# Kernel tuning notes

Hardware: AMD Instinct MI355X
Metric: run time of the kernel (lower is better)

## Reference

```python
import jax, jax.numpy as jnp
import numpy as np

IMAGE_MAX_DIM = 1024
POOL = 7
NUM_CLASSES = 81
N_ROIS = 2000
BN_EPS = 1e-3


def _make_boxes(key, n):
    k1, k2, k3, k4 = jax.random.split(key, 4)
    cx = jax.random.uniform(k1, (n,), minval=0.0, maxval=IMAGE_MAX_DIM)
    cy = jax.random.uniform(k2, (n,), minval=0.0, maxval=IMAGE_MAX_DIM)
    w = jax.random.uniform(k3, (n,), minval=16.0, maxval=512.0)
    h = jax.random.uniform(k4, (n,), minval=16.0, maxval=512.0)
    x1 = jnp.clip(cx - w / 2, 0.0, IMAGE_MAX_DIM - 2.0)
    y1 = jnp.clip(cy - h / 2, 0.0, IMAGE_MAX_DIM - 2.0)
    x2 = jnp.clip(cx + w / 2, x1 + 1.0, IMAGE_MAX_DIM)
    y2 = jnp.clip(cy + h / 2, y1 + 1.0, IMAGE_MAX_DIM)
    return jnp.stack([x1, y1, x2, y2], axis=-1)[None]  # [1, n, 4]


def setup_inputs() -> dict:
    key = jax.random.key(0)
    ks = jax.random.split(key, 16)
    d = {
        'p2': jax.random.normal(ks[0], (1, 256, 256, 256), jnp.float32),
        'p3': jax.random.normal(ks[1], (1, 256, 128, 128), jnp.float32),
        'p4': jax.random.normal(ks[2], (1, 256, 64, 64), jnp.float32),
        'p5': jax.random.normal(ks[3], (1, 256, 32, 32), jnp.float32),
        'rpn_rois': _make_boxes(ks[4], N_ROIS),
        'conv1_w': jax.random.normal(ks[5], (1024, 256, POOL, POOL), jnp.float32) * 0.02,
        'conv1_b': jnp.zeros((1024,), jnp.float32),
        'bn1_g': jnp.ones((1024,), jnp.float32),
        'bn1_b': jnp.zeros((1024,), jnp.float32),
        'bn1_m': jnp.zeros((1024,), jnp.float32),
        'bn1_v': jnp.ones((1024,), jnp.float32),
        'conv2_w': jax.random.normal(ks[6], (1024, 1024), jnp.float32) * 0.02,
        'conv2_b': jnp.zeros((1024,), jnp.float32),
        'bn2_g': jnp.ones((1024,), jnp.float32),
        'bn2_b': jnp.zeros((1024,), jnp.float32),
        'bn2_m': jnp.zeros((1024,), jnp.float32),
        'bn2_v': jnp.ones((1024,), jnp.float32),
        'logits_w': jax.random.normal(ks[7], (NUM_CLASSES, 1024), jnp.float32) * 0.02,
        'logits_b': jnp.zeros((NUM_CLASSES,), jnp.float32),
        'bbox_w': jax.random.normal(ks[8], (NUM_CLASSES * 4, 1024), jnp.float32) * 0.02,
        'bbox_b': jnp.zeros((NUM_CLASSES * 4,), jnp.float32),
    }
    return d


def _crop_resize(fmap, boxes):
    """TF-style crop_and_resize, bilinear. fmap [C,H,W]; boxes [N,4] = (y1,x1,y2,x2) normalized."""
    C, H, W = fmap.shape
    dt = fmap.dtype
    y1, x1, y2, x2 = boxes[:, 0], boxes[:, 1], boxes[:, 2], boxes[:, 3]
    t = (jnp.arange(POOL, dtype=dt) / (POOL - 1))  # [P]
    ys = y1[:, None] * (H - 1) + t[None, :] * ((y2 - y1) * (H - 1))[:, None]  # [N,P]
    xs = x1[:, None] * (W - 1) + t[None, :] * ((x2 - x1) * (W - 1))[:, None]  # [N,P]
    y0 = jnp.floor(ys)
    x0 = jnp.floor(xs)
    ly = (ys - y0)[None, :, :, None]  # [1,N,P,1]
    lx = (xs - x0)[None, :, None, :]  # [1,N,1,P]
    y0i = jnp.clip(y0.astype(jnp.int32), 0, H - 1)
    y1i = jnp.clip(y0i + 1, 0, H - 1)
    x0i = jnp.clip(x0.astype(jnp.int32), 0, W - 1)
    x1i = jnp.clip(x0i + 1, 0, W - 1)

    def g(yi, xi):  # -> [C,N,P,P]
        return fmap[:, yi[:, :, None], xi[:, None, :]]

    out = (g(y0i, x0i) * (1 - ly) * (1 - lx) + g(y0i, x1i) * (1 - ly) * lx
           + g(y1i, x0i) * ly * (1 - lx) + g(y1i, x1i) * ly * lx)
    return jnp.transpose(out, (1, 0, 2, 3))  # [N,C,P,P]


def _forward(p2, p3, p4, p5, rpn_rois, conv1_w, conv1_b, bn1_g, bn1_b, bn1_m, bn1_v,
             conv2_w, conv2_b, bn2_g, bn2_b, bn2_m, bn2_v, logits_w, logits_b, bbox_w, bbox_b):
    rois = rpn_rois.reshape(-1, 4)  # [N,4] (x1,y1,x2,y2) in pixels
    x1, y1, x2, y2 = rois[:, 0], rois[:, 1], rois[:, 2], rois[:, 3]
    # level = clamp(round(log2(sqrt(area)/224)) + 4, 2, 5)
    roi_level = jnp.clip(jnp.round(jnp.log2(jnp.sqrt((y2 - y1) * (x2 - x1)) / 224.0)) + 4.0, 2.0, 5.0)
    boxes_n = (rois / float(IMAGE_MAX_DIM))[:, [1, 0, 3, 2]]  # (y1,x1,y2,x2) normalized

    pooled = jnp.zeros((rois.shape[0], 256, POOL, POOL), rois.dtype)
    for lvl, fmap in zip(range(2, 6), [p2, p3, p4, p5]):
        crops = _crop_resize(fmap[0], boxes_n)  # [N,256,P,P]
        mask = (roi_level == float(lvl))[:, None, None, None]
        pooled = pooled + jnp.where(mask, crops, 0.0)

    # conv1: 7x7 valid conv over [N,256,7,7] -> [N,1024]
    h = jnp.einsum('nchw,ochw->no', pooled, conv1_w) + conv1_b
    h = (h - bn1_m) * jax.lax.rsqrt(bn1_v + BN_EPS) * bn1_g + bn1_b
    h = jax.nn.relu(h)
    # conv2: 1x1 conv == matmul
    h = h @ conv2_w.T + conv2_b
    h = (h - bn2_m) * jax.lax.rsqrt(bn2_v + BN_EPS) * bn2_g + bn2_b
    shared = jax.nn.relu(h)  # [N,1024]

    logits = shared @ logits_w.T + logits_b
    probs = jax.nn.softmax(logits, axis=-1)
    bbox = shared @ bbox_w.T + bbox_b
    return (logits.reshape(1, N_ROIS, NUM_CLASSES),
            probs.reshape(1, N_ROIS, NUM_CLASSES),
            bbox.reshape(1, N_ROIS, NUM_CLASSES, 4))


def reference(p2, p3, p4, p5, rpn_rois, conv1_w, conv1_b, bn1_g, bn1_b, bn1_m, bn1_v,
              conv2_w, conv2_b, bn2_g, bn2_b, bn2_m, bn2_v, logits_w, logits_b, bbox_w, bbox_b):
    return _forward(p2, p3, p4, p5, rpn_rois, conv1_w, conv1_b, bn1_g, bn1_b, bn1_m, bn1_v,
                    conv2_w, conv2_b, bn2_g, bn2_b, bn2_m, bn2_v, logits_w, logits_b, bbox_w, bbox_b)
```

## Files before the change

### kernel.cpp

```cpp
#include <hip/hip_runtime.h>
#include <stdint.h>

#define NROI 2000
#define MPAD 2048
#define KP   12544
#define N1   1024
#define NCLS 81
#define NBOX 324
#define N3   405
#define N3P  448
#define BN_EPS 0.001f
#define KSPLIT 8

typedef __attribute__((ext_vector_type(8))) short bf16x8;
typedef __attribute__((ext_vector_type(4))) float f32x4;
typedef __attribute__((ext_vector_type(8))) unsigned short u16x8;

__device__ inline unsigned short f2bf(float f) {
  union { float f; unsigned u; } v; v.f = f;
  unsigned r = v.u + 0x7fffu + ((v.u >> 16) & 1u);
  return (unsigned short)(r >> 16);
}

__device__ inline float bf2f(unsigned short h) {
  union { unsigned u; float f; } v; v.u = (unsigned)h << 16; return v.f;
}

__device__ inline void gld16(const unsigned short* g, unsigned short* l) {
  __builtin_amdgcn_global_load_lds(
      (const __attribute__((address_space(1))) void*)g,
      (__attribute__((address_space(3))) void*)l, 16, 0, 0);
}

__device__ __forceinline__ void kslice(int kz, int& off, int& len) {
  if (kz < 4) { off = kz * 1536; len = 1536; }
  else        { off = 6144 + (kz - 4) * 1600; len = 1600; }
}

__global__ __launch_bounds__(256) void front_t(
    const float* __restrict__ p2, const float* __restrict__ p3,
    const float* __restrict__ p4, const float* __restrict__ p5,
    unsigned short* __restrict__ f2t, unsigned short* __restrict__ f3t,
    unsigned short* __restrict__ f4t, unsigned short* __restrict__ f5t) {
  int bb2 = blockIdx.x;
  int t = threadIdx.x;
  const float* src;
  unsigned short* dst;
  int HW;
  if (bb2 < 1024)      { src = p2; dst = f2t; HW = 65536; }
  else if (bb2 < 1280) { bb2 -= 1024; src = p3; dst = f3t; HW = 16384; }
  else if (bb2 < 1344) { bb2 -= 1280; src = p4; dst = f4t; HW = 4096; }
  else                 { bb2 -= 1344; src = p5; dst = f5t; HW = 1024; }
  int p0 = bb2 * 64;
  int lane = t & 63, w = t >> 6;
  int pq = (lane & 15) * 4;
  int cg = (lane >> 4) * 8;
#pragma unroll
  for (int it = 0; it < 2; ++it) {
    int c = w * 64 + it * 32 + cg;
    const float* sp = src + (size_t)c * HW + p0 + pq;
    float4 v[8];
#pragma unroll
    for (int k = 0; k < 8; ++k)
      v[k] = *(const float4*)(sp + (size_t)k * HW);
    unsigned short* dp = dst + (size_t)(p0 + pq) * 256 + c;
    u16x8 o0, o1, o2, o3;
#pragma unroll
    for (int k = 0; k < 8; ++k) {
      o0[k] = f2bf(v[k].x);
      o1[k] = f2bf(v[k].y);
      o2[k] = f2bf(v[k].z);
      o3[k] = f2bf(v[k].w);
    }
    *(u16x8*)(dp)       = o0;
    *(u16x8*)(dp + 256) = o1;
    *(u16x8*)(dp + 512) = o2;
    *(u16x8*)(dp + 768) = o3;
  }
}

__global__ __launch_bounds__(256) void roi_prep(
    const unsigned short* __restrict__ f2t, const unsigned short* __restrict__ f3t,
    const unsigned short* __restrict__ f4t, const unsigned short* __restrict__ f5t,
    const float* __restrict__ rois, unsigned short* __restrict__ pooled,
    const float* __restrict__ c1w, const float* __restrict__ c2w,
    const float* __restrict__ lw, const float* __restrict__ bw,
    const float* c1b, const float* g1, const float* b1, const float* m1, const float* v1,
    const float* c2b, const float* g2, const float* b2, const float* m2, const float* v2,
    const float* lb, const float* bb,
    unsigned short* __restrict__ w1p, unsigned short* __restrict__ w2b,
    unsigned short* __restrict__ w3b,
    float* s1, float* t1, float* s2, float* t2, float* b3) {
  __shared__ unsigned short srep[6272];
  int b = blockIdx.x;
  int t = threadIdx.x;
  if (b < 2048) {
    int n = b;
    int lane = t & 63, w = t >> 6;
    int c0 = lane * 4;
    unsigned short* out = pooled + (size_t)n * KP;
    if (n >= NROI) {
      for (int p = w; p < 49; p += 4)
        *(ushort4*)(out + p * 256 + c0) = make_ushort4(0, 0, 0, 0);
      return;
    }
    float x1 = rois[n * 4 + 0], y1 = rois[n * 4 + 1];
    float x2 = rois[n * 4 + 2], y2 = rois[n * 4 + 3];
    float area = (y2 - y1) * (x2 - x1);
    float lvl_f = rintf(log2f(sqrtf(area) / 224.0f)) + 4.0f;
    lvl_f = fminf(fmaxf(lvl_f, 2.0f), 5.0f);
    int lvl = (int)lvl_f;
    const unsigned short* f;
    int H;
    if (lvl == 2)      { f = f2t; H = 256; }
    else if (lvl == 3) { f = f3t; H = 128; }
    else if (lvl == 4) { f = f4t; H = 64;  }
    else               { f = f5t; H = 32;  }
    int W = H;
    const float inv = 1.0f / 1024.0f;
    float yn1 = y1 * inv, xn1 = x1 * inv, yn2 = y2 * inv, xn2 = x2 * inv;
    float hs = (yn2 - yn1) * (H - 1);
    float ws = (xn2 - xn1) * (W - 1);
    float yb = yn1 * (H - 1);
    float xb = xn1 * (W - 1);

    for (int p = w; p < 49; p += 4) {
      int py = p / 7, px = p - py * 7;
      float ysv = yb + ((float)py / 6.0f) * hs;
      float xsv = xb + ((float)px / 6.0f) * ws;
      float y0f = floorf(ysv), x0f = floorf(xsv);
      float ly = ysv - y0f, lx = xsv - x0f;
      int y0 = min(max((int)y0f, 0), H - 1);
      int y1i = min(y0 + 1, H - 1);
      int x0 = min(max((int)x0f, 0), W - 1);
      int x1i = min(x0 + 1, W - 1);
      ushort4 v00 = *(const ushort4*)(f + ((size_t)y0 * W + x0) * 256 + c0);
      ushort4 v01 = *(const ushort4*)(f + ((size_t)y0 * W + x1i) * 256 + c0);
      ushort4 v10 = *(const ushort4*)(f + ((size_t)y1i * W + x0) * 256 + c0);
      ushort4 v11 = *(const ushort4*)(f + ((size_t)y1i * W + x1i) * 256 + c0);
      ushort4 o;
      {
        float a = bf2f(v00.x), bq = bf2f(v01.x), cq = bf2f(v10.x), d = bf2f(v11.x);
        float top = a + lx * (bq - a), bot = cq + lx * (d - cq);
        o.x = f2bf(top + ly * (bot - top));
      }
      {
        float a = bf2f(v00.y), bq = bf2f(v01.y), cq = bf2f(v10.y), d = bf2f(v11.y);
        float top = a + lx * (bq - a), bot = cq + lx * (d - cq);
        o.y = f2bf(top + ly * (bot - top));
      }
      {
        float a = bf2f(v00.z), bq = bf2f(v01.z), cq = bf2f(v10.z), d = bf2f(v11.z);
        float top = a + lx * (bq - a), bot = cq + lx * (d - cq);
        o.z = f2bf(top + ly * (bot - top));
      }
      {
        float a = bf2f(v00.w), bq = bf2f(v01.w), cq = bf2f(v10.w), d = bf2f(v11.w);
        float top = a + lx * (bq - a), bot = cq + lx * (d - cq);
        o.w = f2bf(top + ly * (bot - top));
      }
      *(ushort4*)(out + p * 256 + c0) = o;
    }
  } else if (b < 4096) {
    int idx = b - 2048;
    int o = idx >> 1, h = idx & 1;
    const float4* src = (const float4*)(c1w + (size_t)o * KP + h * 6272);
    for (int k = t; k < 1568; k += 256) {
      float4 v = src[k];
      ushort4 q;
      q.x = f2bf(v.x); q.y = f2bf(v.y); q.z = f2bf(v.z); q.w = f2bf(v.w);
      *(ushort4*)&srep[k * 4] = q;
    }
    __syncthreads();
    unsigned short* dst = w1p + (size_t)o * KP + h * 128;
    int ch4 = (t & 31) * 4;
    int jw = t >> 5;
    for (int j = jw; j < 49; j += 8) {
      ushort4 q;
      q.x = srep[(ch4 + 0) * 49 + j];
      q.y = srep[(ch4 + 1) * 49 + j];
      q.z = srep[(ch4 + 2) * 49 + j];
      q.w = srep[(ch4 + 3) * 49 + j];
      *(ushort4*)(dst + j * 256 + ch4) = q;
    }
  } else if (b < 5120) {
    int j4 = (b - 4096) * 256 + t;
    float4 v = ((const float4*)c2w)[j4];
    ushort4 q;
    q.x = f2bf(v.x); q.y = f2bf(v.y); q.z = f2bf(v.z); q.w = f2bf(v.w);
    *(ushort4*)(w2b + (size_t)j4 * 4) = q;
  } else if (b < 5568) {
    int row = b - 5120;
    int k = t * 4;
    float4 v = {0.f, 0.f, 0.f, 0.f};
    if (row < NCLS)      v = *(const float4*)(lw + (size_t)row * 1024 + k);
    else if (row < N3)   v = *(const float4*)(bw + (size_t)(row - NCLS) * 1024 + k);
    ushort4 q;
    q.x = f2bf(v.x); q.y = f2bf(v.y); q.z = f2bf(v.z); q.w = f2bf(v.w);
    *(ushort4*)(w3b + (size_t)row * 1024 + k) = q;
  } else {
    for (int i = t; i < 1024; i += 256) {
      float sc = g1[i] * rsqrtf(v1[i] + BN_EPS);
      s1[i] = sc;
      t1[i] = (c1b[i] - m1[i]) * sc + b1[i];
      float ss = g2[i] * rsqrtf(v2[i] + BN_EPS);
      s2[i] = ss;
      t2[i] = (c2b[i] - m2[i]) * ss + b2[i];
    }
    for (int i = t; i < N3P; i += 256)
      b3[i] = (i < NCLS) ? lb[i] : (i < N3 ? bb[i - NCLS] : 0.0f);
  }
}

__global__ __launch_bounds__(512, 2) void gemm1_sk3(
    const unsigned short* __restrict__ A, const unsigned short* __restrict__ B,
    unsigned short* __restrict__ part) {
  __shared__ unsigned short AsF[4 * 8192];
  __shared__ unsigned short BsF[4 * 8192];
  int bid = blockIdx.x;
  int kz = bid & 7;
  int u = bid >> 3;
  int bn0 = (u & 3) * 256;
  int bm0 = (u >> 2) * 256;
  int koff, klen;
  kslice(kz, koff, klen);
  int nph = klen >> 5;

  int t = threadIdx.x;
  int lane = t & 63, w = t >> 6;
  int wr = w >> 2, wc = w & 3;
  int ln = lane & 15, q = lane >> 4;

  int clog = (lane & 3) ^ ((lane >> 3) & 3);
  int l4 = lane >> 2;
  const unsigned short* gA0 = A + (size_t)(bm0 + w * 32 + l4) * KP + koff + clog * 8;
  const unsigned short* gA1 = gA0 + (size_t)16 * KP;
  const unsigned short* gB0 = B + (size_t)(bn0 + w * 32 + l4) * KP + koff + clog * 8;
  const unsigned short* gB1 = gB0 + (size_t)16 * KP;
  int dc0 = (w * 128 + lane) * 8;
  int dc1 = dc0 + 64 * 8;

  int rxor = (q ^ ((ln >> 1) & 3)) * 8;
  int rdA = (wr * 128 + ln) * 32 + rxor;
  int rdB = (wc * 64 + ln) * 32 + rxor;

  f32x4 acc[8][4] = {};

#pragma unroll
  for (int ph = 0; ph < 3; ++ph) {
    int src = ph * 32;
    int db = ph * 8192;
    gld16(gA0 + src, AsF + db + dc0);
    gld16(gA1 + src, AsF + db + dc1);
    gld16(gB0 + src, BsF + db + dc0);
    gld16(gB1 + src, BsF + db + dc1);
  }
  asm volatile("s_waitcnt vmcnt(8)" ::: "memory");
  __builtin_amdgcn_s_barrier();
  asm volatile("" ::: "memory");

  for (int ph = 0; ph < nph; ++ph) {
    int rb = (ph & 3) * 8192;
    bf16x8 af[8], bfr[4];
#pragma unroll
    for (int mi = 0; mi < 8; ++mi)
      af[mi] = *(const bf16x8*)&AsF[rb + rdA + mi * 512];
#pragma unroll
    for (int nj = 0; nj < 4; ++nj)
      bfr[nj] = *(const bf16x8*)&BsF[rb + rdB + nj * 512];

    int phn = ph + 3;
    int src = (phn < nph) ? phn * 32 : 0;
    int db = (phn & 3) * 8192;
    gld16(gA0 + src, AsF + db + dc0);
    gld16(gA1 + src, AsF + db + dc1);
    gld16(gB0 + src, BsF + db + dc0);
    gld16(gB1 + src, BsF + db + dc1);

    __builtin_amdgcn_s_setprio(1);
#pragma unroll
    for (int mi = 0; mi < 8; ++mi)
#pragma unroll
      for (int nj = 0; nj < 4; ++nj)
        acc[mi][nj] = __builtin_amdgcn_mfma_f32_16x16x32_bf16(
            af[mi], bfr[nj], acc[mi][nj], 0, 0, 0);
    __builtin_amdgcn_s_setprio(0);

    asm volatile("s_waitcnt vmcnt(8)" ::: "memory");
    __builtin_amdgcn_s_barrier();
    asm volatile("" ::: "memory");
  }

  asm volatile("s_waitcnt vmcnt(0)" ::: "memory");

  unsigned short* po = part + (size_t)kz * MPAD * N1;
#pragma unroll
  for (int mi = 0; mi < 8; ++mi) {
    int m = bm0 + wr * 128 + mi * 16 + q * 4;
#pragma unroll
    for (int nj = 0; nj < 4; ++nj) {
      int n = bn0 + wc * 64 + nj * 16 + ln;
#pragma unroll
      for (int r = 0; r < 4; ++r)
        po[(size_t)(m + r) * N1 + n] = f2bf(acc[mi][nj][r]);
    }
  }
}

__global__ void reduce_sk(const unsigned short* __restrict__ part,
                          const float* __restrict__ sc, const float* __restrict__ sh,
                          unsigned short* __restrict__ outb) {
  const size_t P = (size_t)MPAD * N1;
  int m = blockIdx.x;
  int t = threadIdx.x;
  float4 v = {0.f, 0.f, 0.f, 0.f};
#pragma unroll
  for (int kz = 0; kz < KSPLIT; ++kz) {
    ushort4 u = *(const ushort4*)(part + kz * P + (size_t)m * N1 + t * 4);
    v.x += bf2f(u.x); v.y += bf2f(u.y); v.z += bf2f(u.z); v.w += bf2f(u.w);
  }
  int n0 = t * 4;
  ushort4 o;
  if (m < NROI) {
    o.x = f2bf(fmaxf(v.x * sc[n0 + 0] + sh[n0 + 0], 0.0f));
    o.y = f2bf(fmaxf(v.y * sc[n0 + 1] + sh[n0 + 1], 0.0f));
    o.z = f2bf(fmaxf(v.z * sc[n0 + 2] + sh[n0 + 2], 0.0f));
    o.w = f2bf(fmaxf(v.w * sc[n0 + 3] + sh[n0 + 3], 0.0f));
  } else {
    o = make_ushort4(0, 0, 0, 0);
  }
  *(ushort4*)(outb + (size_t)m * N1 + n0) = o;
}

template <int MODE>
__global__ __launch_bounds__(256) void gemm_bt(
    const unsigned short* __restrict__ A, const unsigned short* __restrict__ B,
    int M, int N, int K,
    const float* __restrict__ sc, const float* __restrict__ sh,
    unsigned short* __restrict__ outb, float* __restrict__ outf,
    int validM, int ldo) {
  __shared__ unsigned short As[64 * 64];
  __shared__ unsigned short Bs[64 * 64];
  int bm0 = blockIdx.y * 64;
  int bn0 = blockIdx.x * 64;
  int t = threadIdx.x;
  int lane = t & 63, w = t >> 6;
  int wm = (w & 1) * 32, wn = (w >> 1) * 32;
  int ln = lane & 15, q = lane >> 4;

  int r8 = t >> 3, j8 = t & 7;
  int sj = j8 ^ (r8 & 7);
  const unsigned short* ga = A + (size_t)(bm0 + r8) * K + sj * 8;
  const unsigned short* gb = B + (size_t)(bn0 + r8) * K + sj * 8;
  unsigned short* la = &As[t * 8];
  unsigned short* lb = &Bs[t * 8];
  int e = ln & 7;

  f32x4 acc00 = {0.f, 0.f, 0.f, 0.f}, acc01 = {0.f, 0.f, 0.f, 0.f};
  f32x4 acc10 = {0.f, 0.f, 0.f, 0.f}, acc11 = {0.f, 0.f, 0.f, 0.f};

  for (int k0 = 0; k0 < K; k0 += 64) {
    gld16(ga + k0, la);
    gld16(ga + k0 + (size_t)32 * K, la + 2048);
    gld16(gb + k0, lb);
    gld16(gb + k0 + (size_t)32 * K, lb + 2048);
    __syncthreads();
#pragma unroll
    for (int h = 0; h < 2; ++h) {
      int slot = ((h * 4 + q) ^ e) * 8;
      bf16x8 a0 = *(const bf16x8*)&As[(wm + ln) * 64 + slot];
      bf16x8 a1 = *(const bf16x8*)&As[(wm + 16 + ln) * 64 + slot];
      bf16x8 b0 = *(const bf16x8*)&Bs[(wn + ln) * 64 + slot];
      bf16x8 b1 = *(const bf16x8*)&Bs[(wn + 16 + ln) * 64 + slot];
      acc00 = __builtin_amdgcn_mfma_f32_16x16x32_bf16(a0, b0, acc00, 0, 0, 0);
      acc01 = __builtin_amdgcn_mfma_f32_16x16x32_bf16(a0, b1, acc01, 0, 0, 0);
      acc10 = __builtin_amdgcn_mfma_f32_16x16x32_bf16(a1, b0, acc10, 0, 0, 0);
      acc11 = __builtin_amdgcn_mfma_f32_16x16x32_bf16(a1, b1, acc11, 0, 0, 0);
    }
    __syncthreads();
  }

  f32x4 accs[2][2] = {{acc00, acc01}, {acc10, acc11}};
#pragma unroll
  for (int i = 0; i < 2; ++i)
#pragma unroll
    for (int j = 0; j < 2; ++j)
#pragma unroll
      for (int r = 0; r < 4; ++r) {
        int m = bm0 + wm + i * 16 + q * 4 + r;
        int n = bn0 + wn + j * 16 + ln;
        float v = accs[i][j][r];
        if (MODE == 1) {
          float o = fmaxf(v * sc[n] + sh[n], 0.0f);
          outb[(size_t)m * ldo + n] = (m < validM) ? f2bf(o) : (unsigned short)0;
        } else {
          outf[(size_t)m * ldo + n] = v + sh[n];
        }
      }
}

__global__ void head(const float* __restrict__ fc3, float* __restrict__ out) {
  int r = blockIdx.x;
  int t = threadIdx.x;
  const float* row = fc3 + (size_t)r * N3P;
  float v0 = (t < NCLS) ? row[t] : -INFINITY;
  float v1 = (t + 64 < NCLS) ? row[t + 64] : -INFINITY;
  float m = fmaxf(v0, v1);
#pragma unroll
  for (int o = 32; o > 0; o >>= 1) m = fmaxf(m, __shfl_xor(m, o, 64));
  float e0 = (t < NCLS) ? expf(v0 - m) : 0.0f;
  float e1 = (t + 64 < NCLS) ? expf(v1 - m) : 0.0f;
  float s = e0 + e1;
#pragma unroll
  for (int o = 32; o > 0; o >>= 1) s += __shfl_xor(s, o, 64);
  float invs = 1.0f / s;
  float* ol = out + (size_t)r * NCLS;
  float* op = out + 162000 + (size_t)r * NCLS;
  float* ob = out + 324000 + (size_t)r * NBOX;
  if (t < NCLS) { ol[t] = v0; op[t] = e0 * invs; }
  if (t + 64 < NCLS) { ol[t + 64] = v1; op[t + 64] = e1 * invs; }
  for (int j = t; j < NBOX; j += 64) ob[j] = row[NCLS + j];
}

extern "C" void kernel_launch(void* const* d_in, const int* in_sizes, int n_in,
                              void* d_out, int out_size, void* d_ws, size_t ws_size,
                              hipStream_t stream) {
  const float* p2  = (const float*)d_in[0];
  const float* p3  = (const float*)d_in[1];
  const float* p4  = (const float*)d_in[2];
  const float* p5  = (const float*)d_in[3];
  const float* roi = (const float*)d_in[4];
  const float* c1w = (const float*)d_in[5];
  const float* c1b = (const float*)d_in[6];
  const float* g1  = (const float*)d_in[7];
  const float* b1  = (const float*)d_in[8];
  const float* m1  = (const float*)d_in[9];
  const float* v1  = (const float*)d_in[10];
  const float* c2w = (const float*)d_in[11];
  const float* c2b = (const float*)d_in[12];
  const float* g2  = (const float*)d_in[13];
  const float* b2  = (const float*)d_in[14];
  const float* m2  = (const float*)d_in[15];
  const float* v2  = (const float*)d_in[16];
  const float* lw  = (const float*)d_in[17];
  const float* lb  = (const float*)d_in[18];
  const float* bw  = (const float*)d_in[19];
  const float* bb  = (const float*)d_in[20];
  float* out = (float*)d_out;

  char* ws = (char*)d_ws;
  size_t off = 0;
  auto alloc = [&](size_t bytes) {
    void* p = ws + off;
    off = (off + bytes + 255) & ~(size_t)255;
    return p;
  };
  unsigned short* pooled = (unsigned short*)alloc((size_t)MPAD * KP * 2);
  unsigned short* w1p    = (unsigned short*)alloc((size_t)N1 * KP * 2);
  unsigned short* w2b    = (unsigned short*)alloc((size_t)N1 * N1 * 2);
  unsigned short* w3b    = (unsigned short*)alloc((size_t)N3P * N1 * 2);
  unsigned short* a2     = (unsigned short*)alloc((size_t)MPAD * N1 * 2);
  unsigned short* shd    = (unsigned short*)alloc((size_t)MPAD * N1 * 2);
  float* fc3 = (float*)alloc((size_t)MPAD * N3P * 4);
  char* ub = (char*)alloc((size_t)48 * 1024 * 1024);
  unsigned short* f2t = (unsigned short*)ub;
  unsigned short* f3t = (unsigned short*)(ub + 33554432);
  unsigned short* f4t = (unsigned short*)(ub + 33554432 + 8388608);
  unsigned short* f5t = (unsigned short*)(ub + 33554432 + 8388608 + 2097152);
  unsigned short* part = (unsigned short*)ub;
  float* s1  = (float*)alloc(1024 * 4);
  float* t1  = (float*)alloc(1024 * 4);
  float* s2  = (float*)alloc(1024 * 4);
  float* t2  = (float*)alloc(1024 * 4);
  float* b3  = (float*)alloc(N3P * 4);

  front_t<<<1360, 256, 0, stream>>>(p2, p3, p4, p5, f2t, f3t, f4t, f5t);

  roi_prep<<<5569, 256, 0, stream>>>(f2t, f3t, f4t, f5t, roi, pooled,
                                     c1w, c2w, lw, bw,
                                     c1b, g1, b1, m1, v1, c2b, g2, b2, m2, v2,
                                     lb, bb,
                                     w1p, w2b, w3b, s1, t1, s2, t2, b3);

  gemm1_sk3<<<256, 512, 0, stream>>>(pooled, w1p, part);
  reduce_sk<<<MPAD, 256, 0, stream>>>(part, s1, t1, a2);

  gemm_bt<1><<<dim3(N1 / 64, MPAD / 64), 256, 0, stream>>>(
      a2, w2b, MPAD, N1, N1, s2, t2, shd, nullptr, NROI, N1);
  gemm_bt<2><<<dim3(N3P / 64, MPAD / 64), 256, 0, stream>>>(
      shd, w3b, MPAD, N3P, N1, nullptr, b3, nullptr, fc3, NROI, N3P);

  head<<<NROI, 64, 0, stream>>>(fc3, out);
}
```

Before: 309.7 us.

## Halve gemm1 M tile and shrink LDS ring to raise occupancy

The split-K conv1 GEMM moves from 256x256 tiles to 128x256 tiles, doubling the grid to 512 blocks. The LDS ring drops from 4 slots with 3-deep prefetch to 3 slots with 2-deep prefetch, and launch bounds ask for 4 blocks per CU. The goal is more resident blocks and better CU coverage across the 256 CUs. In exchange, B tiles are reloaded twice as often, each tile has lower arithmetic intensity, and there is less prefetch slack to hide memory latency.

```diff
diff --git a/kernel.cpp b/kernel.cpp
--- a/kernel.cpp
+++ b/kernel.cpp
@@ -212,16 +212,16 @@
   }
 }
 
-__global__ __launch_bounds__(512, 2) void gemm1_sk3(
+__global__ __launch_bounds__(512, 4) void gemm1_sk5(
     const unsigned short* __restrict__ A, const unsigned short* __restrict__ B,
     unsigned short* __restrict__ part) {
-  __shared__ unsigned short AsF[4 * 8192];
-  __shared__ unsigned short BsF[4 * 8192];
+  __shared__ unsigned short AsF[3 * 4096];
+  __shared__ unsigned short BsF[3 * 8192];
   int bid = blockIdx.x;
   int kz = bid & 7;
   int u = bid >> 3;
   int bn0 = (u & 3) * 256;
-  int bm0 = (u >> 2) * 256;
+  int bm0 = (u >> 2) * 128;
   int koff, klen;
   kslice(kz, koff, klen);
   int nph = klen >> 5;
@@ -231,62 +231,60 @@
   int wr = w >> 2, wc = w & 3;
   int ln = lane & 15, q = lane >> 4;
 
-  int clog = (lane & 3) ^ ((lane >> 3) & 3);
-  int l4 = lane >> 2;
-  const unsigned short* gA0 = A + (size_t)(bm0 + w * 32 + l4) * KP + koff + clog * 8;
-  const unsigned short* gA1 = gA0 + (size_t)16 * KP;
-  const unsigned short* gB0 = B + (size_t)(bn0 + w * 32 + l4) * KP + koff + clog * 8;
-  const unsigned short* gB1 = gB0 + (size_t)16 * KP;
-  int dc0 = (w * 128 + lane) * 8;
-  int dc1 = dc0 + 64 * 8;
+  int clog = (t & 3) ^ ((t >> 3) & 3);
+  int row = t >> 2;
+  const unsigned short* gAa = A + (size_t)(bm0 + row) * KP + koff + clog * 8;
+  const unsigned short* gBa = B + (size_t)(bn0 + row) * KP + koff + clog * 8;
+  const unsigned short* gBb = gBa + (size_t)128 * KP;
+  int dA  = t * 8;
+  int dB0 = t * 8;
+  int dB1 = dB0 + 512 * 8;
 
   int rxor = (q ^ ((ln >> 1) & 3)) * 8;
-  int rdA = (wr * 128 + ln) * 32 + rxor;
+  int rdA = (wr * 64 + ln) * 32 + rxor;
   int rdB = (wc * 64 + ln) * 32 + rxor;
 
-  f32x4 acc[8][4] = {};
-
-#pragma unroll
-  for (int ph = 0; ph < 3; ++ph) {
+  f32x4 acc[4][4] = {};
+
+#pragma unroll
+  for (int ph = 0; ph < 2; ++ph) {
     int src = ph * 32;
-    int db = ph * 8192;
-    gld16(gA0 + src, AsF + db + dc0);
-    gld16(gA1 + src, AsF + db + dc1);
-    gld16(gB0 + src, BsF + db + dc0);
-    gld16(gB1 + src, BsF + db + dc1);
-  }
-  asm volatile("s_waitcnt vmcnt(8)" ::: "memory");
+    gld16(gAa + src, AsF + ph * 4096 + dA);
+    gld16(gBa + src, BsF + ph * 8192 + dB0);
+    gld16(gBb + src, BsF + ph * 8192 + dB1);
+  }
+  asm volatile("s_waitcnt vmcnt(3)" ::: "memory");
   __builtin_amdgcn_s_barrier();
   asm volatile("" ::: "memory");
 
   for (int ph = 0; ph < nph; ++ph) {
-    int rb = (ph & 3) * 8192;
-    bf16x8 af[8], bfr[4];
-#pragma unroll
-    for (int mi = 0; mi < 8; ++mi)
-      af[mi] = *(const bf16x8*)&AsF[rb + rdA + mi * 512];
+    int sl = ph % 3;
+    int rbA = sl * 4096, rbB = sl * 8192;
+    bf16x8 af[4], bfr[4];
+#pragma unroll
+    for (int mi = 0; mi < 4; ++mi)
+      af[mi] = *(const bf16x8*)&AsF[rbA + rdA + mi * 512];
 #pragma unroll
     for (int nj = 0; nj < 4; ++nj)
-      bfr[nj] = *(const bf16x8*)&BsF[rb + rdB + nj * 512];
-
-    int phn = ph + 3;
+      bfr[nj] = *(const bf16x8*)&BsF[rbB + rdB + nj * 512];
+
+    int phn = ph + 2;
     int src = (phn < nph) ? phn * 32 : 0;
-    int db = (phn & 3) * 8192;
-    gld16(gA0 + src, AsF + db + dc0);
-    gld16(gA1 + src, AsF + db + dc1);
-    gld16(gB0 + src, BsF + db + dc0);
-    gld16(gB1 + src, BsF + db + dc1);
+    int sn = phn % 3;
+    gld16(gAa + src, AsF + sn * 4096 + dA);
+    gld16(gBa + src, BsF + sn * 8192 + dB0);
+    gld16(gBb + src, BsF + sn * 8192 + dB1);
 
     __builtin_amdgcn_s_setprio(1);
 #pragma unroll
-    for (int mi = 0; mi < 8; ++mi)
+    for (int mi = 0; mi < 4; ++mi)
 #pragma unroll
       for (int nj = 0; nj < 4; ++nj)
         acc[mi][nj] = __builtin_amdgcn_mfma_f32_16x16x32_bf16(
             af[mi], bfr[nj], acc[mi][nj], 0, 0, 0);
     __builtin_amdgcn_s_setprio(0);
 
-    asm volatile("s_waitcnt vmcnt(8)" ::: "memory");
+    asm volatile("s_waitcnt vmcnt(3)" ::: "memory");
     __builtin_amdgcn_s_barrier();
     asm volatile("" ::: "memory");
   }
@@ -295,8 +293,8 @@
 
   unsigned short* po = part + (size_t)kz * MPAD * N1;
 #pragma unroll
-  for (int mi = 0; mi < 8; ++mi) {
-    int m = bm0 + wr * 128 + mi * 16 + q * 4;
+  for (int mi = 0; mi < 4; ++mi) {
+    int m = bm0 + wr * 64 + mi * 16 + q * 4;
 #pragma unroll
     for (int nj = 0; nj < 4; ++nj) {
       int n = bn0 + wc * 64 + nj * 16 + ln;
@@ -482,7 +480,7 @@
                                      lb, bb,
                                      w1p, w2b, w3b, s1, t1, s2, t2, b3);
 
-  gemm1_sk3<<<256, 512, 0, stream>>>(pooled, w1p, part);
+  gemm1_sk5<<<512, 512, 0, stream>>>(pooled, w1p, part);
   reduce_sk<<<MPAD, 256, 0, stream>>>(part, s1, t1, a2);
 
   gemm_bt<1><<<dim3(N1 / 64, MPAD / 64), 256, 0, stream>>>(
```

Result: no change. 314.9 us (+1.7%).
